# Performance work log

Measured on AMD Instinct MI355X. Metric: run time of the kernel, lower is better.

Reference implementation:

```python
import jax, jax.numpy as jnp
import numpy as np

B, T, C, H = 2, 2048, 1024, 16
D = C // H  # head dim = 64


def setup_inputs() -> dict:
    key = jax.random.key(0)
    ks = jax.random.split(key, 9)
    x = jax.random.normal(ks[0], (B, T, C), dtype=jnp.float32)
    # causal mask: True above the diagonal => positions to mask out
    mask = jnp.triu(jnp.ones((T, T), dtype=bool), k=1)[None, None]  # [1,1,T,T]
    s = 0.02
    Wq = jax.random.normal(ks[1], (C, C), dtype=jnp.float32) * s
    Wk = jax.random.normal(ks[2], (C, C), dtype=jnp.float32) * s
    Wv = jax.random.normal(ks[3], (C, C), dtype=jnp.float32) * s
    Wo = jax.random.normal(ks[4], (C, C), dtype=jnp.float32) * s
    bq = jax.random.normal(ks[5], (C,), dtype=jnp.float32) * s
    bk = jax.random.normal(ks[6], (C,), dtype=jnp.float32) * s
    bv = jax.random.normal(ks[7], (C,), dtype=jnp.float32) * s
    bo = jax.random.normal(ks[8], (C,), dtype=jnp.float32) * s
    return {"x": x, "mask": mask, "Wq": Wq, "bq": bq, "Wk": Wk, "bk": bk,
            "Wv": Wv, "bv": bv, "Wo": Wo, "bo": bo}


def reference(x, mask, Wq, bq, Wk, bk, Wv, bv, Wo, bo):
    b, t, c = x.shape
    # QKV projections, split heads -> [B,H,T,D]
    q = (x @ Wq + bq).reshape(b, t, H, D).transpose(0, 2, 1, 3)
    k = (x @ Wk + bk).reshape(b, t, H, D).transpose(0, 2, 1, 3)
    v = (x @ Wv + bv).reshape(b, t, H, D).transpose(0, 2, 1, 3)
    # scaled dot-product scores [B,H,T,T]
    att = jnp.einsum('bhtd,bhsd->bhts', q, k) * (1.0 / jnp.sqrt(jnp.float32(D)))
    att = jnp.where(mask, jnp.float32(-jnp.inf), att)
    att = jax.nn.softmax(att, axis=-1)  # dropout p=0.0 -> identity
    y = jnp.einsum('bhts,bhsd->bhtd', att, v)  # [B,H,T,D]
    y = y.transpose(0, 2, 1, 3).reshape(b, t, c)
    return y @ Wo + bo
```

## Files before the change

kernel.cpp:

```cpp
#include <hip/hip_runtime.h>
#include <hip/hip_bf16.h>

#define BB 2
#define TT 2048
#define CC 1024
#define HH 16
#define DD 64
#define MM (BB*TT)

typedef float f32x4 __attribute__((ext_vector_type(4)));
typedef __bf16 bf16x8 __attribute__((ext_vector_type(8)));
typedef unsigned int u32x4 __attribute__((ext_vector_type(4)));
typedef unsigned int u32x2 __attribute__((ext_vector_type(2)));

__device__ __forceinline__ unsigned short f2bf(float f) {
    unsigned int u = __float_as_uint(f);
    u += 0x7fff + ((u >> 16) & 1);
    return (unsigned short)(u >> 16);
}
__device__ __forceinline__ unsigned int pk2(float a, float b) {
    return (unsigned int)f2bf(a) | ((unsigned int)f2bf(b) << 16);
}

__device__ __forceinline__ void gload_lds16(const void* g, void* l) {
    __builtin_amdgcn_global_load_lds(
        (const __attribute__((address_space(1))) unsigned int*)(unsigned long long)g,
        (__attribute__((address_space(3))) unsigned int*)(unsigned int)(unsigned long long)l,
        16, 0, 0);
}

__global__ __launch_bounds__(256) void cvt_f32_bf16(
    const float* __restrict__ in, unsigned short* __restrict__ out)
{
    const size_t i = (size_t)blockIdx.x * 256 + threadIdx.x;
    const float4* in4 = (const float4*)in;
    float4 a = in4[2 * i], b = in4[2 * i + 1];
    u32x4 o;
    o[0] = pk2(a.x, a.y); o[1] = pk2(a.z, a.w);
    o[2] = pk2(b.x, b.y); o[3] = pk2(b.z, b.w);
    *(u32x4*)(out + 8 * i) = o;
}

__global__ __launch_bounds__(256) void wtrans_kernel(
    const float* __restrict__ W0, const float* __restrict__ W1,
    const float* __restrict__ W2, const float* __restrict__ W3,
    unsigned short* __restrict__ wt)
{
    const int tid = threadIdx.x;
    const int n0 = blockIdx.x * 64;
    const int k0 = blockIdx.y * 64;
    const int which = blockIdx.z;
    const float* W = (which == 0) ? W0 : (which == 1) ? W1 : (which == 2) ? W2 : W3;

    __shared__ float t_lds[64][68];

    #pragma unroll
    for (int p = 0; p < 4; ++p) {
        int idx = tid + p * 256;
        int r   = idx >> 4;
        int c4  = (idx & 15) * 4;
        *(float4*)&t_lds[r][c4] = *(const float4*)(W + (size_t)(k0 + r) * CC + n0 + c4);
    }
    __syncthreads();

    const int nl = tid >> 2;
    const int ks = (tid & 3) * 16;
    unsigned int w[8];
    #pragma unroll
    for (int j = 0; j < 8; ++j)
        w[j] = pk2(t_lds[ks + 2 * j][nl], t_lds[ks + 2 * j + 1][nl]);
    unsigned short* dst = wt + (size_t)which * CC * CC + (size_t)(n0 + nl) * CC + k0 + ks;
    u32x4 o0; o0[0] = w[0]; o0[1] = w[1]; o0[2] = w[2]; o0[3] = w[3];
    u32x4 o1; o1[0] = w[4]; o1[1] = w[5]; o1[2] = w[6]; o1[3] = w[7];
    *(u32x4*)dst = o0;
    *(u32x4*)(dst + 8) = o1;
}

__global__ __launch_bounds__(256) void gemm_qkv_mfma(
    const unsigned short* __restrict__ xbf, const unsigned short* __restrict__ wt,
    const float* __restrict__ bq, const float* __restrict__ bk, const float* __restrict__ bv,
    unsigned short* __restrict__ qbf, unsigned short* __restrict__ kbf,
    unsigned short* __restrict__ vtbf)
{
    const int tid = threadIdx.x;
    const int m0 = blockIdx.y * 128;
    const int nc0 = blockIdx.x * 128;
    const int which = nc0 >> 10;
    const int cb = nc0 & 1023;
    const unsigned short* Bt = wt + (size_t)which * CC * CC;
    const float* bias = (which == 0) ? bq : (which == 1) ? bk : bv;

    __shared__ __align__(16) unsigned short lds_a[128][32];
    __shared__ __align__(16) unsigned short lds_b[128][32];
    __shared__ __align__(16) unsigned short ebuf[128][136];

    const int lane = tid & 63;
    const int wv = tid >> 6;
    const int wm = (wv & 1) * 64;
    const int wn = (wv >> 1) * 64;
    const int fr = lane & 15;
    const int ks = lane >> 4;

    const int lrow = lane >> 2;
    const int lcol = (lane & 3) * 8;

    f32x4 acc[4][4];
    #pragma unroll
    for (int i = 0; i < 4; ++i)
        #pragma unroll
        for (int j = 0; j < 4; ++j) { acc[i][j][0]=0.f; acc[i][j][1]=0.f; acc[i][j][2]=0.f; acc[i][j][3]=0.f; }

    for (int k0 = 0; k0 < CC; k0 += 32) {
        __syncthreads();
        #pragma unroll
        for (int c = 0; c < 2; ++c) {
            const int r0 = (wv * 2 + c) * 16;
            gload_lds16(xbf + (size_t)(m0 + r0 + lrow) * CC + k0 + lcol, &lds_a[r0][0]);
            gload_lds16(Bt  + (size_t)(cb + r0 + lrow) * CC + k0 + lcol, &lds_b[r0][0]);
        }
        __syncthreads();

        bf16x8 af[4], bfv[4];
        #pragma unroll
        for (int i = 0; i < 4; ++i) {
            af[i]  = __builtin_bit_cast(bf16x8, *(const u32x4*)&lds_a[wm + i * 16 + fr][ks * 8]);
            bfv[i] = __builtin_bit_cast(bf16x8, *(const u32x4*)&lds_b[wn + i * 16 + fr][ks * 8]);
        }
        #pragma unroll
        for (int mi = 0; mi < 4; ++mi)
            #pragma unroll
            for (int ni = 0; ni < 4; ++ni)
                acc[mi][ni] = __builtin_amdgcn_mfma_f32_16x16x32_bf16(af[mi], bfv[ni], acc[mi][ni], 0, 0, 0);
    }

    if (which != 2) {
        const float scl = (which == 0) ? 0.125f : 1.0f;
        #pragma unroll
        for (int ni = 0; ni < 4; ++ni) {
            const int c_l = wn + ni * 16 + fr;
            const float bv2 = bias[cb + c_l];
            #pragma unroll
            for (int mi = 0; mi < 4; ++mi)
                #pragma unroll
                for (int j = 0; j < 4; ++j)
                    ebuf[wm + mi * 16 + ks * 4 + j][c_l] = f2bf((acc[mi][ni][j] + bv2) * scl);
        }
        __syncthreads();
        unsigned short* dst = (which == 0) ? qbf : kbf;
        #pragma unroll
        for (int p = 0; p < 8; ++p) {
            const int chunk = tid + p * 256;
            const int m_l = chunk >> 4;
            const int c_l8 = (chunk & 15) * 8;
            const int m = m0 + m_l;
            const int b = m >> 11, t = m & 2047;
            const int c = cb + c_l8;
            const int h = c >> 6, d = c & 63;
            *(u32x4*)(dst + (((size_t)(b * HH + h) * TT + t) * DD) + d) =
                *(const u32x4*)&ebuf[m_l][c_l8];
        }
    } else {
        #pragma unroll
        for (int ni = 0; ni < 4; ++ni) {
            const int c_l = wn + ni * 16 + fr;
            const float bv2 = bias[cb + c_l];
            #pragma unroll
            for (int mi = 0; mi < 4; ++mi) {
                const int m_l = wm + mi * 16 + ks * 4;
                unsigned int* q2 = (unsigned int*)&ebuf[c_l][m_l];
                q2[0] = pk2(acc[mi][ni][0] + bv2, acc[mi][ni][1] + bv2);
                q2[1] = pk2(acc[mi][ni][2] + bv2, acc[mi][ni][3] + bv2);
            }
        }
        __syncthreads();
        #pragma unroll
        for (int p = 0; p < 8; ++p) {
            const int chunk = tid + p * 256;
            const int c_l = chunk >> 4;
            const int t_l8 = (chunk & 15) * 8;
            const int c = cb + c_l;
            const int h = c >> 6, d = c & 63;
            const int b = m0 >> 11, t = (m0 & 2047) + t_l8;
            *(u32x4*)(vtbf + ((size_t)(b * HH + h) * DD + d) * TT + t) =
                *(const u32x4*)&ebuf[c_l][t_l8];
        }
    }
}

__global__ __launch_bounds__(512) void attn_mfma(
    const unsigned short* __restrict__ qbf, const unsigned short* __restrict__ kbf,
    const unsigned short* __restrict__ vtbf, unsigned short* __restrict__ ybf)
{
    const int tid  = threadIdx.x;
    const int w    = tid >> 6;
    const int lane = tid & 63;
    const int g    = lane >> 4;
    const int i    = lane & 15;
    const int qi   = 15 - (int)blockIdx.x;
    const int h    = blockIdx.y;
    const int b    = blockIdx.z;
    const int q0   = qi * 128;
    const size_t hq = (size_t)(b * HH + h) * TT * DD;
    const size_t hv = (size_t)(b * HH + h) * DD * TT;

    __shared__ __align__(16) unsigned short k_lds[64][72];
    __shared__ __align__(16) unsigned short vt_lds[64][72];
    __shared__ __align__(16) unsigned short p_lds[128][72];

    bf16x8 qf[2];
    {
        const unsigned short* qrow = qbf + hq + (size_t)(q0 + 16 * w + i) * DD + g * 8;
        qf[0] = __builtin_bit_cast(bf16x8, *(const u32x4*)qrow);
        qf[1] = __builtin_bit_cast(bf16x8, *(const u32x4*)(qrow + 32));
    }

    f32x4 o_acc[4];
    f32x4 m_i, l_i;
    #pragma unroll
    for (int ni = 0; ni < 4; ++ni) { o_acc[ni][0]=0.f; o_acc[ni][1]=0.f; o_acc[ni][2]=0.f; o_acc[ni][3]=0.f; }
    #pragma unroll
    for (int e = 0; e < 4; ++e) { m_i[e] = -1e30f; l_i[e] = 0.f; }

    const int srow  = tid >> 3;
    const int sslot = (tid & 7) * 8;

    const int nt = 2 * qi + 2;
    u32x4 kreg = *(const u32x4*)(kbf + hq + (size_t)srow * DD + sslot);
    u32x4 vreg = *(const u32x4*)(vtbf + hv + (size_t)srow * TT + sslot);

    for (int kk = 0; kk < nt; ++kk) {
        __syncthreads();
        *(u32x4*)&k_lds[srow][sslot]  = kreg;
        *(u32x4*)&vt_lds[srow][sslot] = vreg;
        __syncthreads();
        if (kk + 1 < nt) {
            const int s1 = (kk + 1) * 64;
            kreg = *(const u32x4*)(kbf + hq + (size_t)(s1 + srow) * DD + sslot);
            vreg = *(const u32x4*)(vtbf + hv + (size_t)srow * TT + s1 + sslot);
        }

        if (kk == nt - 1 && w < 4) continue;

        const int s0 = kk * 64;
        f32x4 s_acc[4];
        #pragma unroll
        for (int ni = 0; ni < 4; ++ni) { s_acc[ni][0]=0.f; s_acc[ni][1]=0.f; s_acc[ni][2]=0.f; s_acc[ni][3]=0.f; }
        #pragma unroll
        for (int lks = 0; lks < 2; ++lks)
            #pragma unroll
            for (int ni = 0; ni < 4; ++ni) {
                bf16x8 kb = __builtin_bit_cast(bf16x8,
                    *(const u32x4*)&k_lds[ni * 16 + i][lks * 32 + g * 8]);
                s_acc[ni] = __builtin_amdgcn_mfma_f32_16x16x32_bf16(qf[lks], kb, s_acc[ni], 0, 0, 0);
            }

        if (kk >= 2 * qi) {
            const int r_glob = q0 + 16 * w + 4 * g;
            #pragma unroll
            for (int ni = 0; ni < 4; ++ni) {
                const int s_glob = s0 + ni * 16 + i;
                #pragma unroll
                for (int reg = 0; reg < 4; ++reg)
                    if (s_glob > r_glob + reg) s_acc[ni][reg] = -1e30f;
            }
        }

        f32x4 rmax = s_acc[0];
        #pragma unroll
        for (int ni = 1; ni < 4; ++ni)
            #pragma unroll
            for (int e = 0; e < 4; ++e) rmax[e] = fmaxf(rmax[e], s_acc[ni][e]);
        #pragma unroll
        for (int msk = 1; msk < 16; msk <<= 1)
            #pragma unroll
            for (int e = 0; e < 4; ++e) rmax[e] = fmaxf(rmax[e], __shfl_xor(rmax[e], msk));

        f32x4 m_new, alpha;
        #pragma unroll
        for (int e = 0; e < 4; ++e) {
            m_new[e] = fmaxf(m_i[e], rmax[e]);
            alpha[e] = __expf(m_i[e] - m_new[e]);
        }
        f32x4 rsum;
        #pragma unroll
        for (int e = 0; e < 4; ++e) rsum[e] = 0.f;
        #pragma unroll
        for (int ni = 0; ni < 4; ++ni)
            #pragma unroll
            for (int e = 0; e < 4; ++e) {
                float pv = __expf(s_acc[ni][e] - m_new[e]);
                s_acc[ni][e] = pv;
                rsum[e] += pv;
            }
        #pragma unroll
        for (int msk = 1; msk < 16; msk <<= 1)
            #pragma unroll
            for (int e = 0; e < 4; ++e) rsum[e] += __shfl_xor(rsum[e], msk);
        #pragma unroll
        for (int e = 0; e < 4; ++e) {
            l_i[e] = l_i[e] * alpha[e] + rsum[e];
            m_i[e] = m_new[e];
        }
        #pragma unroll
        for (int ni = 0; ni < 4; ++ni)
            #pragma unroll
            for (int e = 0; e < 4; ++e) o_acc[ni][e] *= alpha[e];

        #pragma unroll
        for (int ni = 0; ni < 4; ++ni)
            #pragma unroll
            for (int reg = 0; reg < 4; ++reg)
                p_lds[16 * w + 4 * g + reg][ni * 16 + i] = f2bf(s_acc[ni][reg]);

        #pragma unroll
        for (int lks = 0; lks < 2; ++lks) {
            bf16x8 pa = __builtin_bit_cast(bf16x8,
                *(const u32x4*)&p_lds[16 * w + i][lks * 32 + g * 8]);
            #pragma unroll
            for (int ni = 0; ni < 4; ++ni) {
                bf16x8 vb = __builtin_bit_cast(bf16x8,
                    *(const u32x4*)&vt_lds[ni * 16 + i][lks * 32 + g * 8]);
                o_acc[ni] = __builtin_amdgcn_mfma_f32_16x16x32_bf16(pa, vb, o_acc[ni], 0, 0, 0);
            }
        }
    }

    f32x4 inv;
    #pragma unroll
    for (int e = 0; e < 4; ++e) inv[e] = 1.0f / l_i[e];
    #pragma unroll
    for (int ni = 0; ni < 4; ++ni)
        #pragma unroll
        for (int reg = 0; reg < 4; ++reg)
            ybf[((size_t)b * TT + (q0 + 16 * w + 4 * g + reg)) * CC + h * DD + ni * 16 + i] =
                f2bf(o_acc[ni][reg] * inv[reg]);
}

__global__ __launch_bounds__(256) void gemm_out_mfma(
    const unsigned short* __restrict__ ybf, const unsigned short* __restrict__ wt_o,
    const float* __restrict__ bo, float* __restrict__ out)
{
    const int tid = threadIdx.x;
    const int m0 = blockIdx.y * 128;
    const int n0 = blockIdx.x * 128;

    __shared__ __align__(16) unsigned short lds_a[128][32];
    __shared__ __align__(16) unsigned short lds_b[128][32];

    const int lane = tid & 63;
    const int wv = tid >> 6;
    const int wm = (wv & 1) * 64;
    const int wn = (wv >> 1) * 64;
    const int fr = lane & 15;
    const int ks = lane >> 4;
    const int lrow = lane >> 2;
    const int lcol = (lane & 3) * 8;

    f32x4 acc[4][4];
    #pragma unroll
    for (int i = 0; i < 4; ++i)
        #pragma unroll
        for (int j = 0; j < 4; ++j) { acc[i][j][0]=0.f; acc[i][j][1]=0.f; acc[i][j][2]=0.f; acc[i][j][3]=0.f; }

    for (int k0 = 0; k0 < CC; k0 += 32) {
        __syncthreads();
        #pragma unroll
        for (int c = 0; c < 2; ++c) {
            const int r0 = (wv * 2 + c) * 16;
            gload_lds16(ybf  + (size_t)(m0 + r0 + lrow) * CC + k0 + lcol, &lds_a[r0][0]);
            gload_lds16(wt_o + (size_t)(n0 + r0 + lrow) * CC + k0 + lcol, &lds_b[r0][0]);
        }
        __syncthreads();

        bf16x8 af[4], bfv[4];
        #pragma unroll
        for (int i = 0; i < 4; ++i) {
            af[i]  = __builtin_bit_cast(bf16x8, *(const u32x4*)&lds_a[wm + i * 16 + fr][ks * 8]);
            bfv[i] = __builtin_bit_cast(bf16x8, *(const u32x4*)&lds_b[wn + i * 16 + fr][ks * 8]);
        }
        #pragma unroll
        for (int mi = 0; mi < 4; ++mi)
            #pragma unroll
            for (int ni = 0; ni < 4; ++ni)
                acc[mi][ni] = __builtin_amdgcn_mfma_f32_16x16x32_bf16(af[mi], bfv[ni], acc[mi][ni], 0, 0, 0);
    }

    #pragma unroll
    for (int ni = 0; ni < 4; ++ni) {
        const int n = n0 + wn + ni * 16 + fr;
        const float bv2 = bo[n];
        #pragma unroll
        for (int mi = 0; mi < 4; ++mi) {
            #pragma unroll
            for (int j = 0; j < 4; ++j) {
                const int m = m0 + wm + mi * 16 + ks * 4 + j;
                out[(size_t)m * CC + n] = acc[mi][ni][j] + bv2;
            }
        }
    }
}

extern "C" void kernel_launch(void* const* d_in, const int* in_sizes, int n_in,
                              void* d_out, int out_size, void* d_ws, size_t ws_size,
                              hipStream_t stream) {
    const float* x  = (const float*)d_in[0];
    const float* Wq = (const float*)d_in[2];
    const float* bq = (const float*)d_in[3];
    const float* Wk = (const float*)d_in[4];
    const float* bk = (const float*)d_in[5];
    const float* Wv = (const float*)d_in[6];
    const float* bv = (const float*)d_in[7];
    const float* Wo = (const float*)d_in[8];
    const float* bo = (const float*)d_in[9];
    float* out = (float*)d_out;

    const size_t NE = (size_t)MM * CC;
    unsigned short* xbf  = (unsigned short*)d_ws;
    unsigned short* ybf  = xbf + NE;
    unsigned short* wt   = ybf + NE;
    unsigned short* qbf  = wt + (size_t)4 * CC * CC;
    unsigned short* kbf  = qbf + NE;
    unsigned short* vtbf = kbf + NE;

    cvt_f32_bf16<<<2048, 256, 0, stream>>>(x, xbf);
    wtrans_kernel<<<dim3(16, 16, 4), 256, 0, stream>>>(Wq, Wk, Wv, Wo, wt);
    gemm_qkv_mfma<<<dim3(24, 32), 256, 0, stream>>>(
        xbf, wt, bq, bk, bv, qbf, kbf, vtbf);
    attn_mfma<<<dim3(TT / 128, HH, BB), 512, 0, stream>>>(qbf, kbf, vtbf, ybf);
    gemm_out_mfma<<<dim3(8, 32), 256, 0, stream>>>(
        ybf, wt + (size_t)3 * CC * CC, bo, out);
}
```

Measured before the change: 271.5 us.

## Transpose attention MFMA so each lane owns a query row, halve block size

Recasts the attention kernel to compute S^T = K·Q^T and O^T = V^T·P^T. Each lane then holds a full query row's statistics, so the softmax max/sum reductions need two cross-lane shuffles instead of four per element. P and Y are written as packed 8-byte stores rather than scalar 2-byte stores. Blocks shrink to 64 queries with 256 threads, doubling the grid and removing the idle-warp diagonal tile, at the cost of loading each K/V tile for half as many queries.

```diff
diff --git a/kernel.cpp b/kernel.cpp
--- a/kernel.cpp
+++ b/kernel.cpp
@@ -187,7 +187,7 @@
     }
 }
 
-__global__ __launch_bounds__(512) void attn_mfma(
+__global__ __launch_bounds__(256) void attn_mfma(
     const unsigned short* __restrict__ qbf, const unsigned short* __restrict__ kbf,
     const unsigned short* __restrict__ vtbf, unsigned short* __restrict__ ybf)
 {
@@ -196,16 +196,16 @@
     const int lane = tid & 63;
     const int g    = lane >> 4;
     const int i    = lane & 15;
-    const int qi   = 15 - (int)blockIdx.x;
+    const int qi   = 31 - (int)blockIdx.x;
     const int h    = blockIdx.y;
-    const int b    = blockIdx.z;
-    const int q0   = qi * 128;
-    const size_t hq = (size_t)(b * HH + h) * TT * DD;
-    const size_t hv = (size_t)(b * HH + h) * DD * TT;
+    const int bb   = blockIdx.z;
+    const int q0   = qi * 64;
+    const size_t hq = (size_t)(bb * HH + h) * TT * DD;
+    const size_t hv = (size_t)(bb * HH + h) * DD * TT;
 
     __shared__ __align__(16) unsigned short k_lds[64][72];
     __shared__ __align__(16) unsigned short vt_lds[64][72];
-    __shared__ __align__(16) unsigned short p_lds[128][72];
+    __shared__ __align__(16) unsigned short p_lds[64][72];
 
     bf16x8 qf[2];
     {
@@ -214,126 +214,113 @@
         qf[1] = __builtin_bit_cast(bf16x8, *(const u32x4*)(qrow + 32));
     }
 
-    f32x4 o_acc[4];
-    f32x4 m_i, l_i;
-    #pragma unroll
-    for (int ni = 0; ni < 4; ++ni) { o_acc[ni][0]=0.f; o_acc[ni][1]=0.f; o_acc[ni][2]=0.f; o_acc[ni][3]=0.f; }
-    #pragma unroll
-    for (int e = 0; e < 4; ++e) { m_i[e] = -1e30f; l_i[e] = 0.f; }
-
-    const int srow  = tid >> 3;
-    const int sslot = (tid & 7) * 8;
-
-    const int nt = 2 * qi + 2;
-    u32x4 kreg = *(const u32x4*)(kbf + hq + (size_t)srow * DD + sslot);
-    u32x4 vreg = *(const u32x4*)(vtbf + hv + (size_t)srow * TT + sslot);
+    f32x4 oT[4];
+    #pragma unroll
+    for (int ni = 0; ni < 4; ++ni) { oT[ni][0]=0.f; oT[ni][1]=0.f; oT[ni][2]=0.f; oT[ni][3]=0.f; }
+    float m_i = -1e30f, l_i = 0.0f;
+
+    const int srow = tid >> 2;
+    const int sc0  = (tid & 3) * 8;
+
+    const int nt = qi + 1;
+    u32x4 kreg0 = *(const u32x4*)(kbf + hq + (size_t)srow * DD + sc0);
+    u32x4 kreg1 = *(const u32x4*)(kbf + hq + (size_t)srow * DD + sc0 + 32);
+    u32x4 vreg0 = *(const u32x4*)(vtbf + hv + (size_t)srow * TT + sc0);
+    u32x4 vreg1 = *(const u32x4*)(vtbf + hv + (size_t)srow * TT + sc0 + 32);
 
     for (int kk = 0; kk < nt; ++kk) {
         __syncthreads();
-        *(u32x4*)&k_lds[srow][sslot]  = kreg;
-        *(u32x4*)&vt_lds[srow][sslot] = vreg;
+        *(u32x4*)&k_lds[srow][sc0]       = kreg0;
+        *(u32x4*)&k_lds[srow][sc0 + 32]  = kreg1;
+        *(u32x4*)&vt_lds[srow][sc0]      = vreg0;
+        *(u32x4*)&vt_lds[srow][sc0 + 32] = vreg1;
         __syncthreads();
         if (kk + 1 < nt) {
             const int s1 = (kk + 1) * 64;
-            kreg = *(const u32x4*)(kbf + hq + (size_t)(s1 + srow) * DD + sslot);
-            vreg = *(const u32x4*)(vtbf + hv + (size_t)srow * TT + s1 + sslot);
-        }
-
-        if (kk == nt - 1 && w < 4) continue;
-
-        const int s0 = kk * 64;
-        f32x4 s_acc[4];
-        #pragma unroll
-        for (int ni = 0; ni < 4; ++ni) { s_acc[ni][0]=0.f; s_acc[ni][1]=0.f; s_acc[ni][2]=0.f; s_acc[ni][3]=0.f; }
+            kreg0 = *(const u32x4*)(kbf + hq + (size_t)(s1 + srow) * DD + sc0);
+            kreg1 = *(const u32x4*)(kbf + hq + (size_t)(s1 + srow) * DD + sc0 + 32);
+            vreg0 = *(const u32x4*)(vtbf + hv + (size_t)srow * TT + s1 + sc0);
+            vreg1 = *(const u32x4*)(vtbf + hv + (size_t)srow * TT + s1 + sc0 + 32);
+        }
+
+        f32x4 sT[4];
+        #pragma unroll
+        for (int ni = 0; ni < 4; ++ni) { sT[ni][0]=0.f; sT[ni][1]=0.f; sT[ni][2]=0.f; sT[ni][3]=0.f; }
         #pragma unroll
         for (int lks = 0; lks < 2; ++lks)
             #pragma unroll
             for (int ni = 0; ni < 4; ++ni) {
-                bf16x8 kb = __builtin_bit_cast(bf16x8,
+                bf16x8 ka = __builtin_bit_cast(bf16x8,
                     *(const u32x4*)&k_lds[ni * 16 + i][lks * 32 + g * 8]);
-                s_acc[ni] = __builtin_amdgcn_mfma_f32_16x16x32_bf16(qf[lks], kb, s_acc[ni], 0, 0, 0);
+                sT[ni] = __builtin_amdgcn_mfma_f32_16x16x32_bf16(ka, qf[lks], sT[ni], 0, 0, 0);
             }
 
-        if (kk >= 2 * qi) {
-            const int r_glob = q0 + 16 * w + 4 * g;
-            #pragma unroll
-            for (int ni = 0; ni < 4; ++ni) {
-                const int s_glob = s0 + ni * 16 + i;
+        if (kk == qi) {
+            const int q_l = 16 * w + i;
+            #pragma unroll
+            for (int ni = 0; ni < 4; ++ni)
                 #pragma unroll
                 for (int reg = 0; reg < 4; ++reg)
-                    if (s_glob > r_glob + reg) s_acc[ni][reg] = -1e30f;
+                    if (ni * 16 + 4 * g + reg > q_l) sT[ni][reg] = -1e30f;
+        }
+
+        float tmax = sT[0][0];
+        #pragma unroll
+        for (int ni = 0; ni < 4; ++ni)
+            #pragma unroll
+            for (int e = 0; e < 4; ++e) tmax = fmaxf(tmax, sT[ni][e]);
+        tmax = fmaxf(tmax, __shfl_xor(tmax, 16));
+        tmax = fmaxf(tmax, __shfl_xor(tmax, 32));
+        const float m_new = fmaxf(m_i, tmax);
+        const float alpha = __expf(m_i - m_new);
+        float lsum = 0.f;
+        #pragma unroll
+        for (int ni = 0; ni < 4; ++ni)
+            #pragma unroll
+            for (int e = 0; e < 4; ++e) {
+                float pv = __expf(sT[ni][e] - m_new);
+                sT[ni][e] = pv;
+                lsum += pv;
             }
-        }
-
-        f32x4 rmax = s_acc[0];
-        #pragma unroll
-        for (int ni = 1; ni < 4; ++ni)
-            #pragma unroll
-            for (int e = 0; e < 4; ++e) rmax[e] = fmaxf(rmax[e], s_acc[ni][e]);
-        #pragma unroll
-        for (int msk = 1; msk < 16; msk <<= 1)
-            #pragma unroll
-            for (int e = 0; e < 4; ++e) rmax[e] = fmaxf(rmax[e], __shfl_xor(rmax[e], msk));
-
-        f32x4 m_new, alpha;
-        #pragma unroll
-        for (int e = 0; e < 4; ++e) {
-            m_new[e] = fmaxf(m_i[e], rmax[e]);
-            alpha[e] = __expf(m_i[e] - m_new[e]);
-        }
-        f32x4 rsum;
-        #pragma unroll
-        for (int e = 0; e < 4; ++e) rsum[e] = 0.f;
+        lsum += __shfl_xor(lsum, 16);
+        lsum += __shfl_xor(lsum, 32);
+        l_i = l_i * alpha + lsum;
+        m_i = m_new;
         #pragma unroll
         for (int ni = 0; ni < 4; ++ni)
             #pragma unroll
-            for (int e = 0; e < 4; ++e) {
-                float pv = __expf(s_acc[ni][e] - m_new[e]);
-                s_acc[ni][e] = pv;
-                rsum[e] += pv;
+            for (int e = 0; e < 4; ++e) oT[ni][e] *= alpha;
+
+        #pragma unroll
+        for (int ni = 0; ni < 4; ++ni) {
+            u32x2 pr;
+            pr[0] = pk2(sT[ni][0], sT[ni][1]);
+            pr[1] = pk2(sT[ni][2], sT[ni][3]);
+            *(u32x2*)&p_lds[16 * w + i][ni * 16 + 4 * g] = pr;
+        }
+
+        #pragma unroll
+        for (int lks = 0; lks < 2; ++lks) {
+            bf16x8 pb = __builtin_bit_cast(bf16x8,
+                *(const u32x4*)&p_lds[16 * w + i][lks * 32 + g * 8]);
+            #pragma unroll
+            for (int ni = 0; ni < 4; ++ni) {
+                bf16x8 va = __builtin_bit_cast(bf16x8,
+                    *(const u32x4*)&vt_lds[ni * 16 + i][lks * 32 + g * 8]);
+                oT[ni] = __builtin_amdgcn_mfma_f32_16x16x32_bf16(va, pb, oT[ni], 0, 0, 0);
             }
-        #pragma unroll
-        for (int msk = 1; msk < 16; msk <<= 1)
-            #pragma unroll
-            for (int e = 0; e < 4; ++e) rsum[e] += __shfl_xor(rsum[e], msk);
-        #pragma unroll
-        for (int e = 0; e < 4; ++e) {
-            l_i[e] = l_i[e] * alpha[e] + rsum[e];
-            m_i[e] = m_new[e];
-        }
-        #pragma unroll
-        for (int ni = 0; ni < 4; ++ni)
-            #pragma unroll
-            for (int e = 0; e < 4; ++e) o_acc[ni][e] *= alpha[e];
-
-        #pragma unroll
-        for (int ni = 0; ni < 4; ++ni)
-            #pragma unroll
-            for (int reg = 0; reg < 4; ++reg)
-                p_lds[16 * w + 4 * g + reg][ni * 16 + i] = f2bf(s_acc[ni][reg]);
-
-        #pragma unroll
-        for (int lks = 0; lks < 2; ++lks) {
-            bf16x8 pa = __builtin_bit_cast(bf16x8,
-                *(const u32x4*)&p_lds[16 * w + i][lks * 32 + g * 8]);
-            #pragma unroll
-            for (int ni = 0; ni < 4; ++ni) {
-                bf16x8 vb = __builtin_bit_cast(bf16x8,
-                    *(const u32x4*)&vt_lds[ni * 16 + i][lks * 32 + g * 8]);
-                o_acc[ni] = __builtin_amdgcn_mfma_f32_16x16x32_bf16(pa, vb, o_acc[ni], 0, 0, 0);
-            }
-        }
-    }
-
-    f32x4 inv;
-    #pragma unroll
-    for (int e = 0; e < 4; ++e) inv[e] = 1.0f / l_i[e];
-    #pragma unroll
-    for (int ni = 0; ni < 4; ++ni)
-        #pragma unroll
-        for (int reg = 0; reg < 4; ++reg)
-            ybf[((size_t)b * TT + (q0 + 16 * w + 4 * g + reg)) * CC + h * DD + ni * 16 + i] =
-                f2bf(o_acc[ni][reg] * inv[reg]);
+        }
+    }
+
+    const float inv = 1.0f / l_i;
+    unsigned short* ybase = ybf + ((size_t)bb * TT + (q0 + 16 * w + i)) * CC + h * DD;
+    #pragma unroll
+    for (int ni = 0; ni < 4; ++ni) {
+        u32x2 st;
+        st[0] = pk2(oT[ni][0] * inv, oT[ni][1] * inv);
+        st[1] = pk2(oT[ni][2] * inv, oT[ni][3] * inv);
+        *(u32x2*)(ybase + ni * 16 + 4 * g) = st;
+    }
 }
 
 __global__ __launch_bounds__(256) void gemm_out_mfma(
@@ -426,7 +413,7 @@
     wtrans_kernel<<<dim3(16, 16, 4), 256, 0, stream>>>(Wq, Wk, Wv, Wo, wt);
     gemm_qkv_mfma<<<dim3(24, 32), 256, 0, stream>>>(
         xbf, wt, bq, bk, bv, qbf, kbf, vtbf);
-    attn_mfma<<<dim3(TT / 128, HH, BB), 512, 0, stream>>>(qbf, kbf, vtbf, ybf);
+    attn_mfma<<<dim3(TT / 64, HH, BB), 256, 0, stream>>>(qbf, kbf, vtbf, ybf);
     gemm_out_mfma<<<dim3(8, 32), 256, 0, stream>>>(
         ybf, wt + (size_t)3 * CC * CC, bo, out);
 }
```

Measured after the change: 248.0 us. 8.7% less time.
